# Kernel tuning notes

Measured on AMD Instinct MI355X. Metric: run time of the kernel, lower is better.

Reference implementation:

```python
import jax, jax.numpy as jnp
import numpy as np
from jax import lax

L = 5            # kernel_len
K_SCALE = 1.0    # k
MAX_THIN_ITERS = 128


def _neighbors(x):
    # x: (B,H,W) int32. Returns 8-neighborhood P2..P9 (N,NE,E,SE,S,SW,W,NW), zero-padded border.
    p = jnp.pad(x, ((0, 0), (1, 1), (1, 1)))
    P2 = p[:, :-2, 1:-1]
    P3 = p[:, :-2, 2:]
    P4 = p[:, 1:-1, 2:]
    P5 = p[:, 2:, 2:]
    P6 = p[:, 2:, 1:-1]
    P7 = p[:, 2:, :-2]
    P8 = p[:, 1:-1, :-2]
    P9 = p[:, :-2, :-2]
    return P2, P3, P4, P5, P6, P7, P8, P9


def _thin_substep(img, sub):
    # One Zhang-Suen thinning sub-iteration (parallel thinning; replaces skimage.skeletonize).
    P2, P3, P4, P5, P6, P7, P8, P9 = _neighbors(img)
    seq = (P2, P3, P4, P5, P6, P7, P8, P9, P2)
    A = sum(((seq[i] == 0) & (seq[i + 1] == 1)).astype(jnp.int32) for i in range(8))
    Bc = P2 + P3 + P4 + P5 + P6 + P7 + P8 + P9
    cond = (img == 1) & (Bc >= 2) & (Bc <= 6) & (A == 1)
    if sub == 0:
        cond = cond & (P2 * P4 * P6 == 0) & (P4 * P6 * P8 == 0)
    else:
        cond = cond & (P2 * P4 * P8 == 0) & (P2 * P6 * P8 == 0)
    return jnp.where(cond, 0, img)


def _skeletonize(mask_bool):
    # mask_bool: (B,H,W) bool -> (B,H,W) float32 skeleton (0/1)
    img0 = mask_bool.astype(jnp.int32)

    def cond_fn(state):
        _, it, changed = state
        return changed & (it < MAX_THIN_ITERS)

    def body_fn(state):
        img, it, _ = state
        new = _thin_substep(_thin_substep(img, 0), 1)
        return new, it + 1, jnp.any(new != img)

    final, _, _ = lax.while_loop(cond_fn, body_fn, (img0, jnp.int32(0), jnp.array(True)))
    return final.astype(jnp.float32)


def _conv_same(x, k):
    # x: (B,1,H,W), k: (1,1,kh,kw); 'same' padding matching F.conv2d(padding=(kh//2,kw//2))
    kh, kw = k.shape[-2], k.shape[-1]
    return lax.conv_general_dilated(x, k, (1, 1), [(kh // 2, kh // 2), (kw // 2, kw // 2)],
                                    dimension_numbers=("NCHW", "OIHW", "NCHW"))


def _direction_map(Bs, k1, k10):
    C = _conv_same(Bs, k1)
    C = (C == 2.0).astype(Bs.dtype)
    D = _conv_same(C, k10)
    D = jnp.minimum(D, 10.0)
    return jnp.where(D == 0.0, 1.0, D)


def _weight_map(logits):
    # Mirrors the torch no_grad block: softmax -> threshold -> skeletonize -> 4 direction maps.
    Z = jax.nn.softmax(logits, axis=1)[:, 1]           # (B,H,W)
    A = Z >= 0.5
    Bs = _skeletonize(A)[:, None]                       # (B,1,H,W)
    dt = Bs.dtype
    k_h1 = jnp.ones((1, 1, 1, L), dt)
    k_v1 = jnp.ones((1, 1, L, 1), dt)
    k_d1 = jnp.flip(jnp.eye(L, dtype=dt), 1).reshape(1, 1, L, L)
    k_b1 = jnp.eye(L, dtype=dt).reshape(1, 1, L, L)
    D = (_direction_map(Bs, k_h1, k_h1 * 10.0)
         + _direction_map(Bs, k_v1, k_v1 * 10.0)
         + _direction_map(Bs, k_d1, k_d1 * 10.0)
         + _direction_map(Bs, k_b1, k_b1 * 10.0))
    D = jnp.where(D >= 10.0, 10.0, D)
    D = jnp.where(D == 2.0, 1.0, D)
    return D[:, 0]                                      # (B,H,W)


def setup_inputs() -> dict:
    key = jax.random.key(0)
    k1, k2 = jax.random.split(key)
    logits = jax.random.normal(k1, (4, 2, 1024, 1024), dtype=jnp.float32)
    target = jax.random.randint(k2, (4, 1024, 1024), 0, 2, dtype=jnp.int32)
    return {"logits": logits, "target": target}


def reference(logits, target):
    D = lax.stop_gradient(_weight_map(logits))
    tgt = target.astype(jnp.int32)
    logp = jax.nn.log_softmax(logits, axis=1)
    ce = -jnp.take_along_axis(logp, tgt[:, None], axis=1)[:, 0]   # (B,H,W)
    hw = ce.shape[1] * ce.shape[2]
    loss_per_img = (D * ce).sum(axis=(1, 2)) / hw                 # valid mask is all-ones (no ignore_index)
    return loss_per_img.mean() * K_SCALE
```

## Files before the change

### kernel.cpp

```cpp
#include <hip/hip_runtime.h>
#include <stdint.h>


#define IMG_B 4
#define IMG_H 1024
#define IMG_W 1024
#define HW (IMG_H * IMG_W)
#define NPIX (IMG_B * HW)
#define TPB 256
#define KW 18
#define ROWS 1032
#define IMG_WORDS (KW * ROWS)
#define NW_INT (IMG_B * IMG_H * 16)

#define R_ITERS 32
#define CONE 44
#define NTILES 256
#define TTPB 1024
#define TLW 6
#define TROWS 258
#define TW (TROWS * TLW)

__device__ __forceinline__ uint64_t* wadr(uint64_t* img, int y, int k) {
    return img + (size_t)(y + 4) * KW + (k + 1);
}
__device__ __forceinline__ const uint64_t* wadr(const uint64_t* img, int y, int k) {
    return img + (size_t)(y + 4) * KW + (k + 1);
}

__device__ __forceinline__ uint64_t eq2_5(uint64_t a, uint64_t b, uint64_t c,
                                          uint64_t d, uint64_t e) {
    uint64_t ab = a ^ b;
    uint64_t s1 = ab ^ c;
    uint64_t c1 = (a & b) | (c & ab);
    uint64_t t1 = s1 & d;
    uint64_t s2 = s1 ^ d;
    uint64_t t2 = s2 & e;
    uint64_t s3 = s2 ^ e;
    uint64_t ct = c1 ^ t1;
    uint64_t w2s = ct ^ t2;
    uint64_t w2c = (c1 & t1) | (t2 & ct);
    return ~s3 & w2s & ~w2c;
}

__device__ __forceinline__ uint64_t thin_core(uint64_t nL, uint64_t nC, uint64_t nR,
                                              uint64_t cL, uint64_t cC, uint64_t cR,
                                              uint64_t sL, uint64_t sC, uint64_t sR,
                                              int sub, uint64_t* cond_out) {
    uint64_t P2 = nC, P6 = sC;
    uint64_t P9 = (nC << 1) | (nL >> 63), P3 = (nC >> 1) | (nR << 63);
    uint64_t P8 = (cC << 1) | (cL >> 63), P4 = (cC >> 1) | (cR << 63);
    uint64_t P7 = (sC << 1) | (sL >> 63), P5 = (sC >> 1) | (sR << 63);

    uint64_t sa = P2 ^ P3, ca = P2 & P3;
    uint64_t sb = P4 ^ P5, cb = P4 & P5;
    uint64_t sc2 = P6 ^ P7, cc2 = P6 & P7;
    uint64_t sd = P8 ^ P9, cd = P8 & P9;
    uint64_t t0x = sa & sb, u0 = sa ^ sb;
    uint64_t v0x = ca ^ cb, v0 = v0x ^ t0x;
    uint64_t w0 = (ca & cb) | (t0x & v0x);
    uint64_t t1x = sc2 & sd, u1 = sc2 ^ sd;
    uint64_t v1x = cc2 ^ cd, v1 = v1x ^ t1x;
    uint64_t w1 = (cc2 & cd) | (t1x & v1x);
    uint64_t b0 = u0 ^ u1, g0 = u0 & u1;
    uint64_t b1x = v0 ^ v1, b1 = b1x ^ g0;
    uint64_t g1 = (v0 & v1) | (g0 & b1x);
    uint64_t b2x = w0 ^ w1, b2 = b2x ^ g1;
    uint64_t b3 = (w0 & w1) | (g1 & b2x);
    uint64_t ge2 = b1 | b2 | b3;
    uint64_t le6 = ~(b3 | (b2 & b1 & b0));

    uint64_t t0 = ~P2 & P3, t1 = ~P3 & P4, t2 = ~P4 & P5, t3 = ~P5 & P6;
    uint64_t t4 = ~P6 & P7, t5 = ~P7 & P8, t6 = ~P8 & P9, t7 = ~P9 & P2;
    uint64_t s0 = t0 | t1, d0 = t0 & t1;
    uint64_t s1 = t2 | t3, d1 = t2 & t3;
    uint64_t s2 = t4 | t5, d2 = t4 & t5;
    uint64_t s3 = t6 | t7, d3 = t6 & t7;
    uint64_t sA = s0 | s1, dA = d0 | d1 | (s0 & s1);
    uint64_t sB = s2 | s3, dB = d2 | d3 | (s2 & s3);
    uint64_t any1 = sA | sB;
    uint64_t any2 = dA | dB | (sA & sB);
    uint64_t A1 = any1 & ~any2;

    uint64_t cond = cC & ge2 & le6 & A1;
    if (sub == 0) cond &= ~(P2 & P4 & P6) & ~(P4 & P6 & P8);
    else          cond &= ~(P2 & P4 & P8) & ~(P2 & P6 & P8);
    *cond_out = cond;
    return cC & ~cond;
}

template<int DY, int DX>
__device__ __forceinline__ uint64_t dir_trig_lds(const uint64_t* r, int gy, int gk) {
    uint64_t sh[9];
    uint64_t any = 0;
    #pragma unroll
    for (int j = -4; j <= 4; ++j) {
        const uint64_t* rr = r + j * DY * TLW;
        const int s = j * DX;
        uint64_t w = rr[0], v;
        if (s > 0)      v = (w >> s) | (rr[1] << (64 - s));
        else if (s < 0) v = (w << (-s)) | (rr[-1] >> (64 + s));
        else            v = w;
        sh[j + 4] = v; any |= v;
    }
    if (!any) return 0;
    uint64_t trig = 0;
    #pragma unroll
    for (int o = -2; o <= 2; ++o) {
        uint64_t E = eq2_5(sh[o + 2], sh[o + 3], sh[o + 4], sh[o + 5], sh[o + 6]);
        if (DY != 0) {
            int qy = gy + o * DY;
            if ((unsigned)qy >= (unsigned)IMG_H) E = 0;
        }
        const int s = o * DX;
        if (s < 0)      { if (gk == 0)  E &= (~0ull) << (-s); }
        else if (s > 0) { if (gk == 15) E &= (~0ull) >> s; }
        trig |= E;
    }
    return trig;
}

__global__ __launch_bounds__(TPB) void mask_kernel(const float* __restrict__ logits,
                                                   uint64_t* __restrict__ bitA,
                                                   float* __restrict__ out) {
    const int gtid = blockIdx.x * TPB + threadIdx.x;
    const int gsz = gridDim.x * TPB;
    const int wid = gtid >> 6, lane = gtid & 63, nwv = gsz >> 6;

    if (gtid == 0) *out = 0.0f;
    for (int i = gtid; i < IMG_B * IMG_WORDS; i += gsz) {
        int w = i % IMG_WORDS;
        int row = w / KW, col = w - row * KW;
        if (row < 4 || row >= ROWS - 4 || col == 0 || col == KW - 1)
            bitA[i] = 0;
    }
    for (int w = wid; w < NW_INT; w += nwv) {
        int b = w >> 14, r2 = w & 16383, y = r2 >> 4, k = r2 & 15;
        int rem = (y << 10) + (k << 6) + lane;
        const float* p0 = logits + (size_t)(2 * b) * HW + rem;
        float l0 = p0[0], l1 = p0[HW];
        uint64_t mask = __ballot(l1 >= l0);
        if (lane == 0) *wadr(bitA + (size_t)b * IMG_WORDS, y, k) = mask;
    }
}

__global__ __launch_bounds__(TTPB) void thin_loss_kernel(
        const uint64_t* __restrict__ gin, const float* __restrict__ logits,
        const int* __restrict__ target, float* __restrict__ out) {
    __shared__ uint64_t lbuf[2][TW];
    __shared__ uint64_t wact[4];
    __shared__ float wsum[16];
    const int tile = blockIdx.x;
    const int tx = tile & 7, ty = (tile >> 3) & 7, tb = tile >> 6;

    for (int i = threadIdx.x; i < TW; i += TTPB) {
        int c = i % TLW, rr = i / TLW;
        if (c == 0 || c == TLW - 1 || rr == 0 || rr == TROWS - 1) {
            lbuf[0][i] = 0; lbuf[1][i] = 0;
        }
    }
    if (threadIdx.x < 4)
        wact[threadIdx.x] = (threadIdx.x == 0 || threadIdx.x == 3) ? ~0ull : 0ull;

    const int r = 1 + (int)threadIdx.x / 4, jw = (int)threadIdx.x & 3;
    const int ci = r * TLW + 1 + jw;
    const int gk0 = 2 * tx + jw - 1;
    uint64_t v = 0;
    {
        int gy = ty * 128 + (r - 1) - 64;
        if ((unsigned)gy < (unsigned)IMG_H)
            v = *wadr(gin + (size_t)tb * IMG_WORDS, gy, gk0);
        lbuf[0][ci] = v;
    }
    __syncthreads();

    const int dd = (r < 65) ? (65 - r) : ((r > 192) ? (r - 192) : 0);
    const int d = (dd > 4) ? dd - 4 : 0;
    const int wv = (int)threadIdx.x >> 6;
    const int qb = (int)threadIdx.x >> 4;

    #pragma unroll 1
    for (int it = 0; it < R_ITERS; ++it) {
        {
            const int ss = 2 * it;
            uint64_t m = wact[ss & 3] | wact[(ss + 3) & 3];
            if (it > 0 && m == 0) break;
            uint64_t cond = 0;
            uint64_t winm = (qb == 0) ? (m & 3ull) : ((m >> (qb - 1)) & 7ull);
            if (winm != 0 && (d + ss < CONE)) {
                const uint64_t* cp = lbuf[0] + ci;
                v = thin_core(cp[-7], cp[-6], cp[-5],
                              cp[-1], v,      cp[1],
                              cp[5],  cp[6],  cp[7], 0, &cond);
            }
            lbuf[1][ci] = v;
            if (threadIdx.x == TTPB - 1) wact[(ss + 2) & 3] = 0;
            uint64_t b = __ballot(cond != 0);
            if ((threadIdx.x & 63) == 0 && b) {
                uint64_t bits = ((b & 0x000000000000FFFFull) ? 1ull : 0ull)
                              | ((b & 0x00000000FFFF0000ull) ? 2ull : 0ull)
                              | ((b & 0x0000FFFF00000000ull) ? 4ull : 0ull)
                              | ((b & 0xFFFF000000000000ull) ? 8ull : 0ull);
                atomicOr((unsigned long long*)&wact[(ss + 1) & 3],
                         (unsigned long long)(bits << (4 * wv)));
            }
            __syncthreads();
        }
        {
            const int ss = 2 * it + 1;
            uint64_t m = wact[ss & 3] | wact[(ss + 3) & 3];
            uint64_t cond = 0;
            uint64_t winm = (qb == 0) ? (m & 3ull) : ((m >> (qb - 1)) & 7ull);
            if (winm != 0 && (d + ss < CONE)) {
                const uint64_t* cp = lbuf[1] + ci;
                v = thin_core(cp[-7], cp[-6], cp[-5],
                              cp[-1], v,      cp[1],
                              cp[5],  cp[6],  cp[7], 1, &cond);
            }
            lbuf[0][ci] = v;
            if (threadIdx.x == TTPB - 1) wact[(ss + 2) & 3] = 0;
            uint64_t b = __ballot(cond != 0);
            if ((threadIdx.x & 63) == 0 && b) {
                uint64_t bits = ((b & 0x000000000000FFFFull) ? 1ull : 0ull)
                              | ((b & 0x00000000FFFF0000ull) ? 2ull : 0ull)
                              | ((b & 0x0000FFFF00000000ull) ? 4ull : 0ull)
                              | ((b & 0xFFFF000000000000ull) ? 8ull : 0ull);
                atomicOr((unsigned long long*)&wact[(ss + 1) & 3],
                         (unsigned long long)(bits << (4 * wv)));
            }
            __syncthreads();
        }
    }

    {
        const int t = (int)threadIdx.x;
        const int w = t >> 2, dirq = t & 3;
        const int rw = 65 + (w >> 1);
        const int cc = 2 + (w & 1);
        const int gy = ty * 128 + (w >> 1);
        const int gk = 2 * tx + (w & 1);
        const uint64_t* bp = &lbuf[0][rw * TLW + cc];
        uint64_t tg;
        if (dirq == 0)      tg = dir_trig_lds<0, 1>(bp, gy, gk);
        else if (dirq == 1) tg = dir_trig_lds<1, 0>(bp, gy, gk);
        else if (dirq == 2) tg = dir_trig_lds<1, 1>(bp, gy, gk);
        else                tg = dir_trig_lds<1, -1>(bp, gy, gk);
        tg |= __shfl_xor(tg, 1);
        tg |= __shfl_xor(tg, 2);

        const int base_rem = (gy << 10) + (gk << 6);
        const float* p0 = logits + (size_t)(2 * tb) * HW + base_rem;
        const float* p1 = p0 + HW;
        const int* pt = target + (size_t)tb * HW + base_rem;
        float acc = 0.0f;
        #pragma unroll
        for (int q = 0; q < 4; ++q) {
            const int px = q * 16 + dirq * 4;
            float4 a = *reinterpret_cast<const float4*>(p0 + px);
            float4 bv = *reinterpret_cast<const float4*>(p1 + px);
            int4 tv = *reinterpret_cast<const int4*>(pt + px);
            unsigned bits4 = (unsigned)(tg >> px) & 0xFu;
            float l0[4] = {a.x, a.y, a.z, a.w};
            float l1[4] = {bv.x, bv.y, bv.z, bv.w};
            int tgt[4] = {tv.x, tv.y, tv.z, tv.w};
            #pragma unroll
            for (int e = 0; e < 4; ++e) {
                float s = tgt[e] ? (l1[e] - l0[e]) : (l0[e] - l1[e]);
                float ce = __logf(1.0f + __expf(-s));
                float wgt = ((bits4 >> e) & 1) ? 10.0f : 4.0f;
                acc += wgt * ce;
            }
        }
        acc *= (1.0f / (float)NPIX);
        #pragma unroll
        for (int off = 32; off > 0; off >>= 1) acc += __shfl_down(acc, off);
        if ((t & 63) == 0) wsum[t >> 6] = acc;
        __syncthreads();
        if (t == 0) {
            float s = 0.0f;
            #pragma unroll
            for (int i2 = 0; i2 < 16; ++i2) s += wsum[i2];
            atomicAdd(out, s);
        }
    }
}

extern "C" void kernel_launch(void* const* d_in, const int* in_sizes, int n_in,
                              void* d_out, int out_size, void* d_ws, size_t ws_size,
                              hipStream_t stream) {
    const float* logits = (const float*)d_in[0];
    const int* target = (const int*)d_in[1];
    float* out = (float*)d_out;
    char* ws = (char*)d_ws;
    uint64_t* bitA = (uint64_t*)(ws + 1024);

    mask_kernel<<<2048, TPB, 0, stream>>>(logits, bitA, out);
    thin_loss_kernel<<<NTILES, TTPB, 0, stream>>>(bitA, logits, target, out);
}
```

Before: 34.78 us.

## Prefetch logits and targets before thinning loop and use LDS-only barriers

Issues the global loads of logits and targets for the loss epilogue before the iterative thinning loop, so their latency overlaps the thinning iterations instead of sitting on the tail. Replaces __syncthreads with a custom barrier that waits only on LDS counters (lgkmcnt) so the in-flight global loads are not drained at each barrier. This holds 48 extra registers per thread across the loop, which may lower occupancy or cause spills in a 1024-thread block.

```diff
diff --git a/kernel.cpp b/kernel.cpp
--- a/kernel.cpp
+++ b/kernel.cpp
@@ -26,6 +26,12 @@
 }
 __device__ __forceinline__ const uint64_t* wadr(const uint64_t* img, int y, int k) {
     return img + (size_t)(y + 4) * KW + (k + 1);
+}
+
+__device__ __forceinline__ void lds_barrier() {
+    asm volatile("s_waitcnt lgkmcnt(0)" ::: "memory");
+    __builtin_amdgcn_s_barrier();
+    asm volatile("" ::: "memory");
 }
 
 __device__ __forceinline__ uint64_t eq2_5(uint64_t a, uint64_t b, uint64_t c,
@@ -170,9 +176,29 @@
         int gy = ty * 128 + (r - 1) - 64;
         if ((unsigned)gy < (unsigned)IMG_H)
             v = *wadr(gin + (size_t)tb * IMG_WORDS, gy, gk0);
-        lbuf[0][ci] = v;
-    }
-    __syncthreads();
+    }
+
+    const int ew = (int)threadIdx.x >> 2, dirq = (int)threadIdx.x & 3;
+    const int egy = ty * 128 + (ew >> 1);
+    const int egk = 2 * tx + (ew & 1);
+    float4 pa[4], pb[4];
+    int4 ptv[4];
+    {
+        const int base_rem = (egy << 10) + (egk << 6);
+        const float* p0 = logits + (size_t)(2 * tb) * HW + base_rem;
+        const float* p1 = p0 + HW;
+        const int* pt = target + (size_t)tb * HW + base_rem;
+        #pragma unroll
+        for (int q = 0; q < 4; ++q) {
+            const int px = q * 16 + dirq * 4;
+            pa[q] = *reinterpret_cast<const float4*>(p0 + px);
+            pb[q] = *reinterpret_cast<const float4*>(p1 + px);
+            ptv[q] = *reinterpret_cast<const int4*>(pt + px);
+        }
+    }
+
+    lbuf[0][ci] = v;
+    lds_barrier();
 
     const int dd = (r < 65) ? (65 - r) : ((r > 192) ? (r - 192) : 0);
     const int d = (dd > 4) ? dd - 4 : 0;
@@ -204,7 +230,7 @@
                 atomicOr((unsigned long long*)&wact[(ss + 1) & 3],
                          (unsigned long long)(bits << (4 * wv)));
             }
-            __syncthreads();
+            lds_barrier();
         }
         {
             const int ss = 2 * it + 1;
@@ -228,41 +254,31 @@
                 atomicOr((unsigned long long*)&wact[(ss + 1) & 3],
                          (unsigned long long)(bits << (4 * wv)));
             }
-            __syncthreads();
+            lds_barrier();
         }
     }
 
     {
         const int t = (int)threadIdx.x;
-        const int w = t >> 2, dirq = t & 3;
-        const int rw = 65 + (w >> 1);
-        const int cc = 2 + (w & 1);
-        const int gy = ty * 128 + (w >> 1);
-        const int gk = 2 * tx + (w & 1);
+        const int rw = 65 + (ew >> 1);
+        const int cc = 2 + (ew & 1);
         const uint64_t* bp = &lbuf[0][rw * TLW + cc];
         uint64_t tg;
-        if (dirq == 0)      tg = dir_trig_lds<0, 1>(bp, gy, gk);
-        else if (dirq == 1) tg = dir_trig_lds<1, 0>(bp, gy, gk);
-        else if (dirq == 2) tg = dir_trig_lds<1, 1>(bp, gy, gk);
-        else                tg = dir_trig_lds<1, -1>(bp, gy, gk);
+        if (dirq == 0)      tg = dir_trig_lds<0, 1>(bp, egy, egk);
+        else if (dirq == 1) tg = dir_trig_lds<1, 0>(bp, egy, egk);
+        else if (dirq == 2) tg = dir_trig_lds<1, 1>(bp, egy, egk);
+        else                tg = dir_trig_lds<1, -1>(bp, egy, egk);
         tg |= __shfl_xor(tg, 1);
         tg |= __shfl_xor(tg, 2);
 
-        const int base_rem = (gy << 10) + (gk << 6);
-        const float* p0 = logits + (size_t)(2 * tb) * HW + base_rem;
-        const float* p1 = p0 + HW;
-        const int* pt = target + (size_t)tb * HW + base_rem;
         float acc = 0.0f;
         #pragma unroll
         for (int q = 0; q < 4; ++q) {
             const int px = q * 16 + dirq * 4;
-            float4 a = *reinterpret_cast<const float4*>(p0 + px);
-            float4 bv = *reinterpret_cast<const float4*>(p1 + px);
-            int4 tv = *reinterpret_cast<const int4*>(pt + px);
             unsigned bits4 = (unsigned)(tg >> px) & 0xFu;
-            float l0[4] = {a.x, a.y, a.z, a.w};
-            float l1[4] = {bv.x, bv.y, bv.z, bv.w};
-            int tgt[4] = {tv.x, tv.y, tv.z, tv.w};
+            float l0[4] = {pa[q].x, pa[q].y, pa[q].z, pa[q].w};
+            float l1[4] = {pb[q].x, pb[q].y, pb[q].z, pb[q].w};
+            int tgt[4] = {ptv[q].x, ptv[q].y, ptv[q].z, ptv[q].w};
             #pragma unroll
             for (int e = 0; e < 4; ++e) {
                 float s = tgt[e] ? (l1[e] - l0[e]) : (l0[e] - l1[e]);
```

Measured after the change: 40.76 us. +17.2%, slower.
